# Kernel optimization log

Hardware: AMD Instinct MI355X
Metric: run time of the kernel (lower is better)

Reference implementation:

```python
import jax, jax.numpy as jnp
import numpy as np

N_NODES = 100000
N_EDGES = 600000
H = 128


def setup_inputs() -> dict:
    key = jax.random.key(0)
    k_z, k_e, k_w1, k_w2 = jax.random.split(key, 4)
    z = jax.random.normal(k_z, (N_NODES, H), dtype=jnp.float32)
    edge_index = jax.random.randint(k_e, (2, N_EDGES), 0, N_NODES, dtype=jnp.int64)
    # Kaiming-ish init scale for the MLP weights
    W1 = jax.random.normal(k_w1, (2 * H, H), dtype=jnp.float32) * (1.0 / np.sqrt(2 * H))
    b1 = jnp.zeros((H,), dtype=jnp.float32)
    W2 = jax.random.normal(k_w2, (H, 1), dtype=jnp.float32) * (1.0 / np.sqrt(H))
    b2 = jnp.zeros((1,), dtype=jnp.float32)
    return {"z": z, "edge_index": edge_index, "W1": W1, "b1": b1, "W2": W2, "b2": b2}


def reference(z, edge_index, W1, b1, W2, b2):
    # Gather source/destination node embeddings: [E, H] each
    src = z[edge_index[0]]
    dst = z[edge_index[1]]
    # Avoid materializing the [E, 2H] concat: split W1 into src/dst blocks
    # so fc1(cat(src,dst)) == src @ W1[:H] + dst @ W1[H:] + b1
    h = src @ W1[:H] + dst @ W1[H:] + b1  # [E, H]
    h = jax.nn.relu(h)
    out = h @ W2 + b2  # [E, 1]
    return out.reshape(-1)
```

## Files before the change

kernel.cpp:

```cpp
#include <hip/hip_runtime.h>
#include <hip/hip_bf16.h>
#include <stdint.h>

#define N_NODES_C 100000
#define N_EDGES_C 600000
#define H_C 128

typedef __bf16 bf16x8 __attribute__((ext_vector_type(8)));
typedef float f32x16 __attribute__((ext_vector_type(16)));
typedef _Float16 half8 __attribute__((ext_vector_type(8)));
typedef unsigned short ushort8 __attribute__((ext_vector_type(8)));

__device__ __forceinline__ unsigned short f2bf(float f) {
    unsigned int u = __builtin_bit_cast(unsigned int, f);
    u += 0x7fffu + ((u >> 16) & 1u);
    return (unsigned short)(u >> 16);
}

__global__ void w1fmt_kernel(const float* __restrict__ W1,
                             unsigned short* __restrict__ w1f) {
    int i = blockIdx.x * blockDim.x + threadIdx.x;
    if (i >= 8 * 8 * 64 * 8) return;
    int j = i & 7;
    int L = (i >> 3) & 63;
    int t = (i >> 9) & 7;
    int s = (i >> 12) & 7;
    int k  = s * 16 + ((L >> 5) * 8) + j;
    int n2 = t * 32 + (L & 31);
    float w = (n2 < 128) ? W1[k * H_C + n2]
                         : W1[(128 + k) * H_C + (n2 - 128)];
    w1f[i] = f2bf(w);
}

__launch_bounds__(256, 2)
__global__ void node_gemm_kernel(const float* __restrict__ z,
                                 const unsigned short* __restrict__ w1f,
                                 const float* __restrict__ b1,
                                 _Float16* __restrict__ uv) {
    const int lane = threadIdx.x & 63;
    const int wv   = threadIdx.x >> 6;
    const int tile = blockIdx.x * 4 + wv;
    if (tile >= N_NODES_C / 32) return;
    const int l31  = lane & 31;
    const int half = lane >> 5;

    const float* arow = z + (size_t)(tile * 32 + l31) * H_C + half * 8;
    f32x16 acc[8] = {};

    #pragma unroll
    for (int s = 0; s < 8; ++s) {
        float4 alo = *reinterpret_cast<const float4*>(arow + s * 16);
        float4 ahi = *reinterpret_cast<const float4*>(arow + s * 16 + 4);
        ushort8 au;
        au[0] = f2bf(alo.x); au[1] = f2bf(alo.y);
        au[2] = f2bf(alo.z); au[3] = f2bf(alo.w);
        au[4] = f2bf(ahi.x); au[5] = f2bf(ahi.y);
        au[6] = f2bf(ahi.z); au[7] = f2bf(ahi.w);
        bf16x8 a = __builtin_bit_cast(bf16x8, au);
        const bf16x8* bp = reinterpret_cast<const bf16x8*>(w1f) + (s * 8) * 64 + lane;
        #pragma unroll
        for (int t = 0; t < 8; ++t) {
            bf16x8 b = bp[t * 64];
            acc[t] = __builtin_amdgcn_mfma_f32_32x32x16_bf16(a, b, acc[t], 0, 0, 0);
        }
    }

    const int node0 = tile * 32;
    #pragma unroll
    for (int t = 0; t < 8; ++t) {
        float badd = (t < 4) ? b1[t * 32 + l31] : 0.0f;
        size_t colbase = (t < 4) ? (size_t)(t * 32 + l31)
                                 : ((size_t)N_NODES_C * H_C + (size_t)((t - 4) * 32 + l31));
        #pragma unroll
        for (int r = 0; r < 16; ++r) {
            int row = (r & 3) + 8 * (r >> 2) + 4 * half;
            float v = acc[t][r] + badd;
            float fother = __shfl_xor(v, 1);
            if ((lane & 1) == 0) {
                unsigned int pk = __builtin_bit_cast(
                    unsigned int, __builtin_amdgcn_cvt_pkrtz(v, fother));
                size_t idx = (size_t)(node0 + row) * H_C + colbase;
                *reinterpret_cast<unsigned int*>(uv + idx) = pk;
            }
        }
    }
}

__global__ void edge_kernel(const _Float16* __restrict__ uv,
                            const int* __restrict__ ei,
                            const float* __restrict__ w2,
                            const float* __restrict__ b2,
                            float* __restrict__ out) {
    const int tid = blockIdx.x * blockDim.x + threadIdx.x;
    const int j   = tid & 15;
    const int q   = tid >> 4;
    const int nq  = (gridDim.x * blockDim.x) >> 4;

    float w2v[8];
    {
        float4 a = *reinterpret_cast<const float4*>(w2 + j * 8);
        float4 b = *reinterpret_cast<const float4*>(w2 + j * 8 + 4);
        w2v[0] = a.x; w2v[1] = a.y; w2v[2] = a.z; w2v[3] = a.w;
        w2v[4] = b.x; w2v[5] = b.y; w2v[6] = b.z; w2v[7] = b.w;
    }
    const float c2 = b2[0];
    const _Float16* vbase = uv + (size_t)N_NODES_C * H_C;

    for (int e = q; e < N_EDGES_C; e += 2 * nq) {
        const int e1 = e + nq;
        const bool has1 = (e1 < N_EDGES_C);
        int s0 = ei[e];
        int d0 = ei[N_EDGES_C + e];
        int s1 = has1 ? ei[e1] : s0;
        int d1 = has1 ? ei[N_EDGES_C + e1] : d0;

        half8 u0 = *reinterpret_cast<const half8*>(uv    + (size_t)s0 * H_C + j * 8);
        half8 v0 = *reinterpret_cast<const half8*>(vbase + (size_t)d0 * H_C + j * 8);
        half8 u1 = *reinterpret_cast<const half8*>(uv    + (size_t)s1 * H_C + j * 8);
        half8 v1 = *reinterpret_cast<const half8*>(vbase + (size_t)d1 * H_C + j * 8);

        float p0 = 0.0f, p1 = 0.0f;
        #pragma unroll
        for (int k = 0; k < 8; ++k) {
            float h0 = (float)u0[k] + (float)v0[k];
            float h1 = (float)u1[k] + (float)v1[k];
            h0 = h0 > 0.0f ? h0 : 0.0f;
            h1 = h1 > 0.0f ? h1 : 0.0f;
            p0 = fmaf(h0, w2v[k], p0);
            p1 = fmaf(h1, w2v[k], p1);
        }
        p0 += __shfl_xor(p0, 1);  p1 += __shfl_xor(p1, 1);
        p0 += __shfl_xor(p0, 2);  p1 += __shfl_xor(p1, 2);
        p0 += __shfl_xor(p0, 4);  p1 += __shfl_xor(p1, 4);
        p0 += __shfl_xor(p0, 8);  p1 += __shfl_xor(p1, 8);
        if (j == 0) {
            out[e] = p0 + c2;
            if (has1) out[e1] = p1 + c2;
        }
    }
}

extern "C" void kernel_launch(void* const* d_in, const int* in_sizes, int n_in,
                              void* d_out, int out_size, void* d_ws, size_t ws_size,
                              hipStream_t stream) {
    const float* z  = (const float*)d_in[0];
    const int*   ei = (const int*)d_in[1];
    const float* W1 = (const float*)d_in[2];
    const float* b1 = (const float*)d_in[3];
    const float* W2 = (const float*)d_in[4];
    const float* b2 = (const float*)d_in[5];
    float* out = (float*)d_out;

    unsigned short* w1f = (unsigned short*)d_ws;
    _Float16* uv = (_Float16*)((char*)d_ws + 65536);

    w1fmt_kernel<<<(8 * 8 * 64 * 8 + 255) / 256, 256, 0, stream>>>(W1, w1f);

    int ntiles = N_NODES_C / 32;
    node_gemm_kernel<<<(ntiles + 3) / 4, 256, 0, stream>>>(z, w1f, b1, uv);

    edge_kernel<<<2048, 256, 0, stream>>>(uv, ei, W2, b2, out);
}
```

Before: 167.6 us.

## Split node GEMM output halves across waves and give each edge group four edges

The node GEMM now assigns each 32-node tile to two waves, one computing the u half and one the v half. This halves the accumulator registers per wave and allows three blocks per CU, at the cost of converting each z tile to bf16 twice. The edge kernel drops the grid-stride loop and launches one 16-lane group per four consecutive edges. Each group loads its indices with int4 reads and issues eight gathers at once, then writes one float4 per group. This is meant to raise memory-level parallelism in the gather, and it relies on the edge count being divisible by four.

New measurement: 162.4 us. -3.1%, faster.

```diff
diff --git a/kernel.cpp b/kernel.cpp
--- a/kernel.cpp
+++ b/kernel.cpp
@@ -32,20 +32,22 @@
     w1f[i] = f2bf(w);
 }
 
-__launch_bounds__(256, 2)
+__launch_bounds__(256, 3)
 __global__ void node_gemm_kernel(const float* __restrict__ z,
                                  const unsigned short* __restrict__ w1f,
                                  const float* __restrict__ b1,
                                  _Float16* __restrict__ uv) {
     const int lane = threadIdx.x & 63;
     const int wv   = threadIdx.x >> 6;
-    const int tile = blockIdx.x * 4 + wv;
-    if (tile >= N_NODES_C / 32) return;
+    const int wid  = blockIdx.x * 4 + wv;
+    if (wid >= 2 * (N_NODES_C / 32)) return;
+    const int tile = wid >> 1;
+    const int uh   = wid & 1;
     const int l31  = lane & 31;
     const int half = lane >> 5;
 
     const float* arow = z + (size_t)(tile * 32 + l31) * H_C + half * 8;
-    f32x16 acc[8] = {};
+    f32x16 acc[4] = {};
 
     #pragma unroll
     for (int s = 0; s < 8; ++s) {
@@ -57,20 +59,21 @@
         au[4] = f2bf(ahi.x); au[5] = f2bf(ahi.y);
         au[6] = f2bf(ahi.z); au[7] = f2bf(ahi.w);
         bf16x8 a = __builtin_bit_cast(bf16x8, au);
-        const bf16x8* bp = reinterpret_cast<const bf16x8*>(w1f) + (s * 8) * 64 + lane;
+        const bf16x8* bp = reinterpret_cast<const bf16x8*>(w1f)
+                           + (s * 8 + uh * 4) * 64 + lane;
         #pragma unroll
-        for (int t = 0; t < 8; ++t) {
+        for (int t = 0; t < 4; ++t) {
             bf16x8 b = bp[t * 64];
             acc[t] = __builtin_amdgcn_mfma_f32_32x32x16_bf16(a, b, acc[t], 0, 0, 0);
         }
     }
 
     const int node0 = tile * 32;
+    const size_t segbase = uh ? (size_t)N_NODES_C * H_C : 0;
     #pragma unroll
-    for (int t = 0; t < 8; ++t) {
-        float badd = (t < 4) ? b1[t * 32 + l31] : 0.0f;
-        size_t colbase = (t < 4) ? (size_t)(t * 32 + l31)
-                                 : ((size_t)N_NODES_C * H_C + (size_t)((t - 4) * 32 + l31));
+    for (int t = 0; t < 4; ++t) {
+        int n = t * 32 + l31;
+        float badd = uh ? 0.0f : b1[n];
         #pragma unroll
         for (int r = 0; r < 16; ++r) {
             int row = (r & 3) + 8 * (r >> 2) + 4 * half;
@@ -79,7 +82,7 @@
             if ((lane & 1) == 0) {
                 unsigned int pk = __builtin_bit_cast(
                     unsigned int, __builtin_amdgcn_cvt_pkrtz(v, fother));
-                size_t idx = (size_t)(node0 + row) * H_C + colbase;
+                size_t idx = segbase + (size_t)(node0 + row) * H_C + n;
                 *reinterpret_cast<unsigned int*>(uv + idx) = pk;
             }
         }
@@ -94,7 +97,8 @@
     const int tid = blockIdx.x * blockDim.x + threadIdx.x;
     const int j   = tid & 15;
     const int q   = tid >> 4;
-    const int nq  = (gridDim.x * blockDim.x) >> 4;
+    const int e0  = q * 4;
+    if (e0 >= N_EDGES_C) return;
 
     float w2v[8];
     {
@@ -106,37 +110,44 @@
     const float c2 = b2[0];
     const _Float16* vbase = uv + (size_t)N_NODES_C * H_C;
 
-    for (int e = q; e < N_EDGES_C; e += 2 * nq) {
-        const int e1 = e + nq;
-        const bool has1 = (e1 < N_EDGES_C);
-        int s0 = ei[e];
-        int d0 = ei[N_EDGES_C + e];
-        int s1 = has1 ? ei[e1] : s0;
-        int d1 = has1 ? ei[N_EDGES_C + e1] : d0;
+    int4 ss = *reinterpret_cast<const int4*>(ei + e0);
+    int4 dd = *reinterpret_cast<const int4*>(ei + N_EDGES_C + e0);
 
-        half8 u0 = *reinterpret_cast<const half8*>(uv    + (size_t)s0 * H_C + j * 8);
-        half8 v0 = *reinterpret_cast<const half8*>(vbase + (size_t)d0 * H_C + j * 8);
-        half8 u1 = *reinterpret_cast<const half8*>(uv    + (size_t)s1 * H_C + j * 8);
-        half8 v1 = *reinterpret_cast<const half8*>(vbase + (size_t)d1 * H_C + j * 8);
+    half8 u0 = *reinterpret_cast<const half8*>(uv    + (size_t)ss.x * H_C + j * 8);
+    half8 v0 = *reinterpret_cast<const half8*>(vbase + (size_t)dd.x * H_C + j * 8);
+    half8 u1 = *reinterpret_cast<const half8*>(uv    + (size_t)ss.y * H_C + j * 8);
+    half8 v1 = *reinterpret_cast<const half8*>(vbase + (size_t)dd.y * H_C + j * 8);
+    half8 u2 = *reinterpret_cast<const half8*>(uv    + (size_t)ss.z * H_C + j * 8);
+    half8 v2 = *reinterpret_cast<const half8*>(vbase + (size_t)dd.z * H_C + j * 8);
+    half8 u3 = *reinterpret_cast<const half8*>(uv    + (size_t)ss.w * H_C + j * 8);
+    half8 v3 = *reinterpret_cast<const half8*>(vbase + (size_t)dd.w * H_C + j * 8);
 
-        float p0 = 0.0f, p1 = 0.0f;
-        #pragma unroll
-        for (int k = 0; k < 8; ++k) {
-            float h0 = (float)u0[k] + (float)v0[k];
-            float h1 = (float)u1[k] + (float)v1[k];
-            h0 = h0 > 0.0f ? h0 : 0.0f;
-            h1 = h1 > 0.0f ? h1 : 0.0f;
-            p0 = fmaf(h0, w2v[k], p0);
-            p1 = fmaf(h1, w2v[k], p1);
-        }
-        p0 += __shfl_xor(p0, 1);  p1 += __shfl_xor(p1, 1);
-        p0 += __shfl_xor(p0, 2);  p1 += __shfl_xor(p1, 2);
-        p0 += __shfl_xor(p0, 4);  p1 += __shfl_xor(p1, 4);
-        p0 += __shfl_xor(p0, 8);  p1 += __shfl_xor(p1, 8);
-        if (j == 0) {
-            out[e] = p0 + c2;
-            if (has1) out[e1] = p1 + c2;
-        }
+    float p0 = 0.0f, p1 = 0.0f, p2 = 0.0f, p3 = 0.0f;
+    #pragma unroll
+    for (int k = 0; k < 8; ++k) {
+        float h0 = (float)u0[k] + (float)v0[k];
+        float h1 = (float)u1[k] + (float)v1[k];
+        float h2 = (float)u2[k] + (float)v2[k];
+        float h3 = (float)u3[k] + (float)v3[k];
+        h0 = h0 > 0.0f ? h0 : 0.0f;
+        h1 = h1 > 0.0f ? h1 : 0.0f;
+        h2 = h2 > 0.0f ? h2 : 0.0f;
+        h3 = h3 > 0.0f ? h3 : 0.0f;
+        p0 = fmaf(h0, w2v[k], p0);
+        p1 = fmaf(h1, w2v[k], p1);
+        p2 = fmaf(h2, w2v[k], p2);
+        p3 = fmaf(h3, w2v[k], p3);
+    }
+    #pragma unroll
+    for (int m = 1; m <= 8; m <<= 1) {
+        p0 += __shfl_xor(p0, m);
+        p1 += __shfl_xor(p1, m);
+        p2 += __shfl_xor(p2, m);
+        p3 += __shfl_xor(p3, m);
+    }
+    if (j == 0) {
+        float4 o = { p0 + c2, p1 + c2, p2 + c2, p3 + c2 };
+        *reinterpret_cast<float4*>(out + e0) = o;
     }
 }
 
@@ -156,8 +167,9 @@
 
     w1fmt_kernel<<<(8 * 8 * 64 * 8 + 255) / 256, 256, 0, stream>>>(W1, w1f);
 
-    int ntiles = N_NODES_C / 32;
-    node_gemm_kernel<<<(ntiles + 3) / 4, 256, 0, stream>>>(z, w1f, b1, uv);
+    int nwaves = 2 * (N_NODES_C / 32);
+    node_gemm_kernel<<<(nwaves + 3) / 4, 256, 0, stream>>>(z, w1f, b1, uv);
 
-    edge_kernel<<<2048, 256, 0, stream>>>(uv, ei, W2, b2, out);
+    int nquarters = N_EDGES_C / 4;
+    edge_kernel<<<(nquarters * 16 + 255) / 256, 256, 0, stream>>>(uv, ei, W2, b2, out);
 }
```
